# Kernel optimization log

Hardware: AMD Instinct MI355X
Metric: run time of the kernel (lower is better)

## Reference

```python
import jax, jax.numpy as jnp
import numpy as np

N_REUPLOADS = 3


def _qrun(x, Wp, bp, W1, b1, W2, b2):
    """Q-RUN layer: linear proj -> sin/cos reupload stack -> tiny per-channel MLP -> flatten.
    x: [..., in_dim]; Wp: [H2, in_dim]; W1: [mlp_h, 2*n_reuploads]; W2: [2, mlp_h].
    Returns [..., 2*H2].
    """
    p = jnp.einsum('...i,hi->...h', x, Wp) + bp                 # [..., H2]
    # features ordered [sin, cos, sin, cos, sin, cos] as in torch.stack of extend-ed list
    sc = jnp.stack([jnp.sin(p), jnp.cos(p)], axis=-1)           # [..., H2, 2]
    feats = jnp.tile(sc, (1,) * (sc.ndim - 1) + (N_REUPLOADS,))  # [..., H2, 6]
    h = jax.nn.relu(jnp.einsum('...k,mk->...m', feats, W1) + b1)  # [..., H2, 32]
    o = jnp.einsum('...m,om->...o', h, W2) + b2                 # [..., H2, 2]
    return o.reshape(o.shape[:-2] + (-1,))                      # flatten(start_dim=-2)


def setup_inputs() -> dict:
    key = jax.random.key(0)
    ks = jax.random.split(key, 20)
    H, I, MH, K = 5120, 27648, 32, 2 * N_REUPLOADS
    d = {}
    d['x'] = jax.random.normal(ks[0], (1, 256, H), dtype=jnp.float32)

    def mk(kbase, in_dim, out_half):
        k1, k2, k3, k4 = jax.random.split(kbase, 4)
        return (
            jax.random.normal(k1, (out_half, in_dim), jnp.float32) * (1.0 / np.sqrt(in_dim)),
            jnp.zeros((out_half,), jnp.float32),
            jax.random.normal(k2, (MH, K), jnp.float32) * 0.1,
            jnp.zeros((MH,), jnp.float32),
            jax.random.normal(k3, (2, MH), jnp.float32) * 0.01,
            jnp.zeros((2,), jnp.float32),
        )

    (d['Wg'], d['bg'], d['W1g'], d['b1g'], d['W2g'], d['b2g']) = mk(ks[1], H, I // 2)
    (d['Wu'], d['bu'], d['W1u'], d['b1u'], d['W2u'], d['b2u']) = mk(ks[2], H, I // 2)
    (d['Wd'], d['bd'], d['W1d'], d['b1d'], d['W2d'], d['b2d']) = mk(ks[3], I, H // 2)
    return d


def reference(x, Wg, bg, W1g, b1g, W2g, b2g,
              Wu, bu, W1u, b1u, W2u, b2u,
              Wd, bd, W1d, b1d, W2d, b2d):
    gate = _qrun(x, Wg, bg, W1g, b1g, W2g, b2g)   # [B,S,27648]
    up = _qrun(x, Wu, bu, W1u, b1u, W2u, b2u)     # [B,S,27648]
    h = jax.nn.silu(gate) * up
    return _qrun(h, Wd, bd, W1d, b1d, W2d, b2d)   # [B,S,5120]
```

## Files before the change

### kernel.cpp

```cpp
#include <hip/hip_runtime.h>
#include <stdint.h>

typedef unsigned short u16;
typedef __attribute__((ext_vector_type(8))) short short8;
typedef __attribute__((ext_vector_type(4))) float f32x4;

#define KGU  5120
#define HCOL 27648
#define NPD  2560
#define KD   27648
#define SPLITD 12
#define KCHD 2304
#define PEL (256*2560)

#define RB4   4
#define ABYT  16384
#define BBYT  16384
#define BUFB  32768

__device__ __forceinline__ void gl_lds16(const void* gp, void* lp) {
  __builtin_amdgcn_global_load_lds((const __attribute__((address_space(1))) uint32_t*)gp,
                                   (__attribute__((address_space(3))) uint32_t*)lp, 16, 0, 0);
}
__device__ __forceinline__ void gl_lds16nt(const void* gp, void* lp) {
  __builtin_amdgcn_global_load_lds((const __attribute__((address_space(1))) uint32_t*)gp,
                                   (__attribute__((address_space(3))) uint32_t*)lp, 16, 0, 2);
}
__device__ __forceinline__ uint32_t f2bf(float x) {
  uint32_t b = __float_as_uint(x);
  return (b + 0x7fffu + ((b >> 16) & 1u)) >> 16;
}
__device__ __forceinline__ uint32_t pk2(float lo, float hi) { return f2bf(lo) | (f2bf(hi) << 16); }
__device__ __forceinline__ float silu(float x) {
  return x * __builtin_amdgcn_rcpf(1.f + __expf(-x));
}
__device__ __forceinline__ short8 mk_bf8(const float4& a, const float4& b) {
  union { uint32_t u[4]; short8 s; } cv;
  cv.u[0] = pk2(a.x, a.y); cv.u[1] = pk2(a.z, a.w);
  cv.u[2] = pk2(b.x, b.y); cv.u[3] = pk2(b.z, b.w);
  return cv.s;
}

__global__ __launch_bounds__(256) void k_cvt(const float* __restrict__ X, u16* __restrict__ Xb) {
  int i = (blockIdx.x * 256 + threadIdx.x) * 8;
  float4 a = *(const float4*)(X + i);
  float4 b = *(const float4*)(X + i + 4);
  uint4 v;
  v.x = pk2(a.x, a.y); v.y = pk2(a.z, a.w); v.z = pk2(b.x, b.y); v.w = pk2(b.z, b.w);
  *(uint4*)(Xb + i) = v;
}

__global__ __launch_bounds__(512, 1)
void k_gu(const u16* __restrict__ X,
          const float* __restrict__ Wg, const float* __restrict__ bg,
          const float* __restrict__ W1g, const float* __restrict__ b1g,
          const float* __restrict__ W2g, const float* __restrict__ b2g,
          const float* __restrict__ Wu, const float* __restrict__ bu,
          const float* __restrict__ W1u, const float* __restrict__ b1u,
          const float* __restrict__ W2u, const float* __restrict__ b2u,
          u16* __restrict__ H) {
  __shared__ __align__(16) char smem[RB4 * BUFB + 1536];
  const int tid = threadIdx.x, lane = tid & 63, wid = tid >> 6;
  const int wm = wid >> 1, wn = wid & 1;
  const int s_ = lane & 15, quad = lane >> 4;
  const int j0 = blockIdx.x * 64;

  float4* mc4 = (float4*)(smem + RB4 * BUFB);
  float*  mc1 = (float*)(smem + RB4 * BUFB + 1024);
  if (tid < 64) {
    int sel = tid >> 5, m = tid & 31;
    const float* w1 = (sel ? W1u : W1g) + m * 6;
    const float* b1 = sel ? b1u : b1g;
    const float* w2 = sel ? W2u : W2g;
    mc4[sel * 32 + m] = make_float4(w1[0] + w1[2] + w1[4], w1[1] + w1[3] + w1[5], b1[m], w2[m]);
    mc1[sel * 32 + m] = w2[32 + m];
  }

  const u16* srcA0 = X + (size_t)(32 * wid + (lane & 15)) * KGU + (lane >> 4) * 8;
  const u16* srcA1 = srcA0 + 16 * KGU;
  const int jrow = j0 + 8 * wid + ((lane & 7) >> 1);
  const float* srcB0 = ((lane & 1) ? Wu : Wg) + (size_t)jrow * KGU + (lane >> 3) * 4;
  const float* srcB1 = srcB0 + 4 * KGU;
  const int dA0 = (2 * wid) * 1024, dA1 = dA0 + 1024;
  const int dB0 = ABYT + (2 * wid) * 1024, dB1 = dB0 + 1024;

  const int aoff0 = wm * 4096 + s_ * 16 + quad * 256;
  const int boff0 = ABYT + wn * 8192 + (s_ >> 3) * 1024 + (s_ & 7) * 16 + quad * 256;

  f32x4 acc[4][4];
#pragma unroll
  for (int i = 0; i < 4; ++i)
#pragma unroll
    for (int j = 0; j < 4; ++j) acc[i][j] = (f32x4)0.f;

  auto stage = [&](int bufb, int t) {
    const int kt = t * 32;
    gl_lds16(srcA0 + kt, smem + bufb + dA0);
    gl_lds16(srcA1 + kt, smem + bufb + dA1);
    gl_lds16nt(srcB0 + kt, smem + bufb + dB0);
    gl_lds16nt(srcB1 + kt, smem + bufb + dB1);
  };
  auto compute = [&](int bufb) {
    const char* base = smem + bufb;
    short8 af[4], bf[4];
#pragma unroll
    for (int mi = 0; mi < 4; ++mi)
      af[mi] = *(const short8*)(base + aoff0 + mi * 1024);
#pragma unroll
    for (int ni = 0; ni < 4; ++ni) {
      float4 f0 = *(const float4*)(base + boff0 + ni * 2048);
      float4 f1 = *(const float4*)(base + boff0 + ni * 2048 + 128);
      bf[ni] = mk_bf8(f0, f1);
    }
    __builtin_amdgcn_s_setprio(1);
#pragma unroll
    for (int mi = 0; mi < 4; ++mi)
#pragma unroll
      for (int ni = 0; ni < 4; ++ni)
        acc[mi][ni] = __builtin_amdgcn_mfma_f32_16x16x32_bf16(af[mi], bf[ni], acc[mi][ni], 0, 0, 0);
    __builtin_amdgcn_s_setprio(0);
  };

  stage(0, 0); stage(BUFB, 1);
#pragma unroll 1
  for (int t = 0; t < 158; ++t) {
    stage(((t + 2) & 3) * BUFB, t + 2);
    asm volatile("s_waitcnt vmcnt(8)" ::: "memory");
    __builtin_amdgcn_s_barrier();
    __builtin_amdgcn_sched_barrier(0);
    compute((t & 3) * BUFB);
  }
  asm volatile("s_waitcnt vmcnt(4)" ::: "memory");
  __builtin_amdgcn_s_barrier();
  __builtin_amdgcn_sched_barrier(0);
  compute((158 & 3) * BUFB);
  asm volatile("s_waitcnt vmcnt(0)" ::: "memory");
  __builtin_amdgcn_s_barrier();
  __builtin_amdgcn_sched_barrier(0);
  compute((159 & 3) * BUFB);

  __syncthreads();
  const int sel = lane & 1;
  const float b2v0 = sel ? b2u[0] : b2g[0];
  const float b2v1 = sel ? b2u[1] : b2g[1];
  const float4* mcs = mc4 + sel * 32;
  const float*  mcw = mc1 + sel * 32;
#pragma unroll
  for (int ni = 0; ni < 4; ++ni) {
    const int c = wn * 64 + ni * 16 + s_;
    const int j = j0 + (c >> 1);
    const float bp = sel ? bu[j] : bg[j];
#pragma unroll
    for (int mi = 0; mi < 4; ++mi) {
      float sv[4], cv[4], o0[4], o1[4];
#pragma unroll
      for (int e = 0; e < 4; ++e) {
        float p = acc[mi][ni][e] + bp;
        sv[e] = __sinf(p); cv[e] = __cosf(p);
        o0[e] = b2v0; o1[e] = b2v1;
      }
#pragma unroll 4
      for (int m = 0; m < 32; ++m) {
        float4 k4 = mcs[m]; float w2b = mcw[m];
#pragma unroll
        for (int e = 0; e < 4; ++e) {
          float hh = fmaxf(fmaf(sv[e], k4.x, fmaf(cv[e], k4.y, k4.z)), 0.f);
          o0[e] = fmaf(hh, k4.w, o0[e]);
          o1[e] = fmaf(hh, w2b, o1[e]);
        }
      }
#pragma unroll
      for (int e = 0; e < 4; ++e) {
        float t0 = __shfl_xor(o0[e], 1);
        float t1 = __shfl_xor(o1[e], 1);
        float g0 = sel ? t0 : o0[e];
        float u0 = sel ? o0[e] : t0;
        float g1 = sel ? t1 : o1[e];
        float u1 = sel ? o1[e] : t1;
        float h0 = silu(g0) * u0, h1 = silu(g1) * u1;
        if (!sel) {
          const int row = wm * 64 + mi * 16 + quad * 4 + e;
          *(uint32_t*)&H[(size_t)row * HCOL + 2 * j] = pk2(h0, h1);
        }
      }
    }
  }
}

__global__ __launch_bounds__(512, 1)
void k_down(const u16* __restrict__ Hb, const float* __restrict__ Wd, float* __restrict__ P2) {
  __shared__ __align__(16) char smem[RB4 * BUFB];
  const int tid = threadIdx.x, lane = tid & 63, wid = tid >> 6;
  const int wm = wid >> 1, wn = wid & 1;
  const int s_ = lane & 15, quad = lane >> 4;
  const int n0 = blockIdx.x * 128;
  const int kc = blockIdx.y * KCHD;

  const u16* srcA0 = Hb + (size_t)(32 * wid + (lane & 15)) * KD + kc + (lane >> 4) * 8;
  const u16* srcA1 = srcA0 + 16 * KD;
  const float* srcB0 = Wd + (size_t)(n0 + 16 * wid + (lane & 7)) * KD + kc + (lane >> 3) * 4;
  const float* srcB1 = srcB0 + 8 * KD;
  const int dA0 = (2 * wid) * 1024, dA1 = dA0 + 1024;
  const int dB0 = ABYT + (2 * wid) * 1024, dB1 = dB0 + 1024;

  const int aoff0 = wm * 4096 + s_ * 16 + quad * 256;
  const int boff0 = ABYT + wn * 8192 + (s_ >> 3) * 1024 + (s_ & 7) * 16 + quad * 256;

  f32x4 acc[4][4];
#pragma unroll
  for (int i = 0; i < 4; ++i)
#pragma unroll
    for (int j = 0; j < 4; ++j) acc[i][j] = (f32x4)0.f;

  auto stage = [&](int bufb, int t) {
    const int kt = t * 32;
    gl_lds16(srcA0 + kt, smem + bufb + dA0);
    gl_lds16(srcA1 + kt, smem + bufb + dA1);
    gl_lds16nt(srcB0 + kt, smem + bufb + dB0);
    gl_lds16nt(srcB1 + kt, smem + bufb + dB1);
  };
  auto compute = [&](int bufb) {
    const char* base = smem + bufb;
    short8 af[4], bf[4];
#pragma unroll
    for (int mi = 0; mi < 4; ++mi)
      af[mi] = *(const short8*)(base + aoff0 + mi * 1024);
#pragma unroll
    for (int ni = 0; ni < 4; ++ni) {
      float4 f0 = *(const float4*)(base + boff0 + ni * 2048);
      float4 f1 = *(const float4*)(base + boff0 + ni * 2048 + 128);
      bf[ni] = mk_bf8(f0, f1);
    }
    __builtin_amdgcn_s_setprio(1);
#pragma unroll
    for (int mi = 0; mi < 4; ++mi)
#pragma unroll
      for (int ni = 0; ni < 4; ++ni)
        acc[mi][ni] = __builtin_amdgcn_mfma_f32_16x16x32_bf16(af[mi], bf[ni], acc[mi][ni], 0, 0, 0);
    __builtin_amdgcn_s_setprio(0);
  };

  stage(0, 0); stage(BUFB, 1);
#pragma unroll 1
  for (int t = 0; t < 70; ++t) {
    stage(((t + 2) & 3) * BUFB, t + 2);
    asm volatile("s_waitcnt vmcnt(8)" ::: "memory");
    __builtin_amdgcn_s_barrier();
    __builtin_amdgcn_sched_barrier(0);
    compute((t & 3) * BUFB);
  }
  asm volatile("s_waitcnt vmcnt(4)" ::: "memory");
  __builtin_amdgcn_s_barrier();
  __builtin_amdgcn_sched_barrier(0);
  compute((70 & 3) * BUFB);
  asm volatile("s_waitcnt vmcnt(0)" ::: "memory");
  __builtin_amdgcn_s_barrier();
  __builtin_amdgcn_sched_barrier(0);
  compute((71 & 3) * BUFB);

  const size_t pb = (size_t)blockIdx.y * PEL;
#pragma unroll
  for (int mi = 0; mi < 4; ++mi) {
    int mrow = wm * 64 + mi * 16 + (quad << 2);
#pragma unroll
    for (int ni = 0; ni < 4; ++ni) {
      int n = n0 + wn * 64 + ni * 16 + s_;
#pragma unroll
      for (int e = 0; e < 4; ++e)
        P2[pb + (size_t)(mrow + e) * NPD + n] = acc[mi][ni][e];
    }
  }
}

__global__ __launch_bounds__(256) void k_fin(const float* __restrict__ P2, const float* __restrict__ bd,
    const float* __restrict__ W1d, const float* __restrict__ b1d, const float* __restrict__ W2d,
    const float* __restrict__ b2d, float* __restrict__ out) {
  __shared__ float4 mc0[32];
  __shared__ float mc1[32];
  const int tid = threadIdx.x;
  if (tid < 32) {
    const float* w = W1d + tid * 6;
    mc0[tid] = make_float4(w[0] + w[2] + w[4], w[1] + w[3] + w[5], b1d[tid], W2d[tid]);
    mc1[tid] = W2d[32 + tid];
  }
  __syncthreads();
  const int idx = blockIdx.x * 256 + tid;
  const int m = idx / NPD, j = idx - m * NPD;
  float p = bd[j];
#pragma unroll
  for (int sk = 0; sk < SPLITD; ++sk) p += P2[(size_t)sk * PEL + idx];
  float s = __sinf(p), c = __cosf(p);
  float o0 = b2d[0], o1 = b2d[1];
#pragma unroll 4
  for (int mm = 0; mm < 32; ++mm) {
    float4 k = mc0[mm];
    float hh = fmaxf(fmaf(s, k.x, fmaf(c, k.y, k.z)), 0.f);
    o0 = fmaf(hh, k.w, o0);
    o1 = fmaf(hh, mc1[mm], o1);
  }
  *(float2*)&out[(size_t)m * 5120 + 2 * j] = make_float2(o0, o1);
}

extern "C" void kernel_launch(void* const* d_in, const int* in_sizes, int n_in,
                              void* d_out, int out_size, void* d_ws, size_t ws_size,
                              hipStream_t stream) {
  const float* x   = (const float*)d_in[0];
  const float* Wg  = (const float*)d_in[1];
  const float* bg  = (const float*)d_in[2];
  const float* W1g = (const float*)d_in[3];
  const float* b1g = (const float*)d_in[4];
  const float* W2g = (const float*)d_in[5];
  const float* b2g = (const float*)d_in[6];
  const float* Wu  = (const float*)d_in[7];
  const float* bu  = (const float*)d_in[8];
  const float* W1u = (const float*)d_in[9];
  const float* b1u = (const float*)d_in[10];
  const float* W2u = (const float*)d_in[11];
  const float* b2u = (const float*)d_in[12];
  const float* Wd  = (const float*)d_in[13];
  const float* bd  = (const float*)d_in[14];
  const float* W1d = (const float*)d_in[15];
  const float* b1d = (const float*)d_in[16];
  const float* W2d = (const float*)d_in[17];
  const float* b2d = (const float*)d_in[18];
  char* ws = (char*)d_ws;
  u16*  xb = (u16*)ws;
  u16*  hb = (u16*)(ws + 2621440);
  float* P2 = (float*)(ws + 16777216);
  if (ws_size < 48234496u) return;

  k_cvt<<<dim3(640), dim3(256), 0, stream>>>(x, xb);
  k_gu<<<dim3(216), dim3(512), 0, stream>>>(xb, Wg, bg, W1g, b1g, W2g, b2g,
                                            Wu, bu, W1u, b1u, W2u, b2u, hb);
  k_down<<<dim3(20, SPLITD), dim3(512), 0, stream>>>(hb, Wd, P2);
  k_fin<<<dim3(2560), dim3(256), 0, stream>>>(P2, bd, W1d, b1d, W2d, b2d, (float*)d_out);
}
```

Measured before the change: 370.3 us.

## Convert fp32 weights to bf16 once in LDS with register-staged double buffering

The GEMM kernels stop copying fp32 weight tiles straight into LDS and converting them to bf16 in every wave. Each thread now loads its weight slice into registers, packs it with v_cvt_pk_bf16_f32, and writes a compact bf16 tile into a 2-stage LDS ring, so all waves share one conversion per element. Blocks shrink to 256 threads over 128 rows with 2 blocks per CU, which doubles the grids and halves LDS per block. The trade-off is a shallower pipeline (2 stages instead of 4) with a full wait on memory and a barrier every iteration, plus weight tiles re-read from memory by twice as many M-split blocks.

```diff
diff --git a/kernel.cpp b/kernel.cpp
--- a/kernel.cpp
+++ b/kernel.cpp
@@ -13,32 +13,25 @@
 #define KCHD 2304
 #define PEL (256*2560)
 
-#define RB4   4
-#define ABYT  16384
-#define BBYT  16384
-#define BUFB  32768
+#define BUF2 16384
+#define BOFF 8192
 
 __device__ __forceinline__ void gl_lds16(const void* gp, void* lp) {
   __builtin_amdgcn_global_load_lds((const __attribute__((address_space(1))) uint32_t*)gp,
                                    (__attribute__((address_space(3))) uint32_t*)lp, 16, 0, 0);
 }
-__device__ __forceinline__ void gl_lds16nt(const void* gp, void* lp) {
-  __builtin_amdgcn_global_load_lds((const __attribute__((address_space(1))) uint32_t*)gp,
-                                   (__attribute__((address_space(3))) uint32_t*)lp, 16, 0, 2);
-}
 __device__ __forceinline__ uint32_t f2bf(float x) {
   uint32_t b = __float_as_uint(x);
   return (b + 0x7fffu + ((b >> 16) & 1u)) >> 16;
 }
 __device__ __forceinline__ uint32_t pk2(float lo, float hi) { return f2bf(lo) | (f2bf(hi) << 16); }
+__device__ __forceinline__ uint32_t cvtpk(float lo, float hi) {
+  uint32_t r;
+  asm("v_cvt_pk_bf16_f32 %0, %1, %2" : "=v"(r) : "v"(lo), "v"(hi));
+  return r;
+}
 __device__ __forceinline__ float silu(float x) {
   return x * __builtin_amdgcn_rcpf(1.f + __expf(-x));
-}
-__device__ __forceinline__ short8 mk_bf8(const float4& a, const float4& b) {
-  union { uint32_t u[4]; short8 s; } cv;
-  cv.u[0] = pk2(a.x, a.y); cv.u[1] = pk2(a.z, a.w);
-  cv.u[2] = pk2(b.x, b.y); cv.u[3] = pk2(b.z, b.w);
-  return cv.s;
 }
 
 __global__ __launch_bounds__(256) void k_cvt(const float* __restrict__ X, u16* __restrict__ Xb) {
@@ -50,7 +43,7 @@
   *(uint4*)(Xb + i) = v;
 }
 
-__global__ __launch_bounds__(512, 1)
+__global__ __launch_bounds__(256, 2)
 void k_gu(const u16* __restrict__ X,
           const float* __restrict__ Wg, const float* __restrict__ bg,
           const float* __restrict__ W1g, const float* __restrict__ b1g,
@@ -59,14 +52,15 @@
           const float* __restrict__ W1u, const float* __restrict__ b1u,
           const float* __restrict__ W2u, const float* __restrict__ b2u,
           u16* __restrict__ H) {
-  __shared__ __align__(16) char smem[RB4 * BUFB + 1536];
+  __shared__ __align__(16) char smem[2 * BUF2 + 1536];
   const int tid = threadIdx.x, lane = tid & 63, wid = tid >> 6;
   const int wm = wid >> 1, wn = wid & 1;
   const int s_ = lane & 15, quad = lane >> 4;
-  const int j0 = blockIdx.x * 64;
-
-  float4* mc4 = (float4*)(smem + RB4 * BUFB);
-  float*  mc1 = (float*)(smem + RB4 * BUFB + 1024);
+  const int m0 = (blockIdx.x & 1) * 128;
+  const int j0 = (blockIdx.x >> 1) * 64;
+
+  float4* mc4 = (float4*)(smem + 2 * BUF2);
+  float*  mc1 = (float*)(smem + 2 * BUF2 + 1024);
   if (tid < 64) {
     int sel = tid >> 5, m = tid & 31;
     const float* w1 = (sel ? W1u : W1g) + m * 6;
@@ -76,16 +70,17 @@
     mc1[sel * 32 + m] = w2[32 + m];
   }
 
-  const u16* srcA0 = X + (size_t)(32 * wid + (lane & 15)) * KGU + (lane >> 4) * 8;
-  const u16* srcA1 = srcA0 + 16 * KGU;
-  const int jrow = j0 + 8 * wid + ((lane & 7) >> 1);
-  const float* srcB0 = ((lane & 1) ? Wu : Wg) + (size_t)jrow * KGU + (lane >> 3) * 4;
-  const float* srcB1 = srcB0 + 4 * KGU;
-  const int dA0 = (2 * wid) * 1024, dA1 = dA0 + 1024;
-  const int dB0 = ABYT + (2 * wid) * 1024, dB1 = dB0 + 1024;
-
-  const int aoff0 = wm * 4096 + s_ * 16 + quad * 256;
-  const int boff0 = ABYT + wn * 8192 + (s_ >> 3) * 1024 + (s_ & 7) * 16 + quad * 256;
+  const int c2 = wid * 2;
+  const u16* srcA0 = X + (size_t)(m0 + c2 * 16 + (lane >> 2)) * KGU + (lane & 3) * 8;
+  const u16* srcA1 = srcA0 + (size_t)16 * KGU;
+  const int dA0 = c2 * 1024, dA1 = dA0 + 1024;
+
+  const int br = tid >> 1, bh = tid & 1;
+  const float* srcB = ((br & 1) ? Wu : Wg) + (size_t)(j0 + (br >> 1)) * KGU + bh * 16;
+  const int bwr = BOFF + br * 64 + bh * 32;
+
+  const int aoff = (wm * 64 + s_) * 64 + quad * 16;
+  const int boff = BOFF + (wn * 64 + s_) * 64 + quad * 16;
 
   f32x4 acc[4][4];
 #pragma unroll
@@ -93,25 +88,33 @@
 #pragma unroll
     for (int j = 0; j < 4; ++j) acc[i][j] = (f32x4)0.f;
 
-  auto stage = [&](int bufb, int t) {
-    const int kt = t * 32;
-    gl_lds16(srcA0 + kt, smem + bufb + dA0);
-    gl_lds16(srcA1 + kt, smem + bufb + dA1);
-    gl_lds16nt(srcB0 + kt, smem + bufb + dB0);
-    gl_lds16nt(srcB1 + kt, smem + bufb + dB1);
-  };
-  auto compute = [&](int bufb) {
-    const char* base = smem + bufb;
+  float4 q0, q1, q2, q3;
+  auto loadB = [&](int kt) {
+    q0 = *(const float4*)(srcB + kt);
+    q1 = *(const float4*)(srcB + kt + 4);
+    q2 = *(const float4*)(srcB + kt + 8);
+    q3 = *(const float4*)(srcB + kt + 12);
+  };
+  auto stageA = [&](int buf, int kt) {
+    gl_lds16(srcA0 + kt, smem + buf + dA0);
+    gl_lds16(srcA1 + kt, smem + buf + dA1);
+  };
+  auto writeB = [&](int buf) {
+    uint4 v0, v1;
+    v0.x = cvtpk(q0.x, q0.y); v0.y = cvtpk(q0.z, q0.w);
+    v0.z = cvtpk(q1.x, q1.y); v0.w = cvtpk(q1.z, q1.w);
+    v1.x = cvtpk(q2.x, q2.y); v1.y = cvtpk(q2.z, q2.w);
+    v1.z = cvtpk(q3.x, q3.y); v1.w = cvtpk(q3.z, q3.w);
+    *(uint4*)(smem + buf + bwr) = v0;
+    *(uint4*)(smem + buf + bwr + 16) = v1;
+  };
+  auto compute = [&](int buf) {
+    const char* base = smem + buf;
     short8 af[4], bf[4];
 #pragma unroll
-    for (int mi = 0; mi < 4; ++mi)
-      af[mi] = *(const short8*)(base + aoff0 + mi * 1024);
-#pragma unroll
-    for (int ni = 0; ni < 4; ++ni) {
-      float4 f0 = *(const float4*)(base + boff0 + ni * 2048);
-      float4 f1 = *(const float4*)(base + boff0 + ni * 2048 + 128);
-      bf[ni] = mk_bf8(f0, f1);
-    }
+    for (int mi = 0; mi < 4; ++mi) af[mi] = *(const short8*)(base + aoff + mi * 1024);
+#pragma unroll
+    for (int ni = 0; ni < 4; ++ni) bf[ni] = *(const short8*)(base + boff + ni * 1024);
     __builtin_amdgcn_s_setprio(1);
 #pragma unroll
     for (int mi = 0; mi < 4; ++mi)
@@ -121,25 +124,31 @@
     __builtin_amdgcn_s_setprio(0);
   };
 
-  stage(0, 0); stage(BUFB, 1);
+  loadB(0); stageA(0, 0);
+  asm volatile("s_waitcnt vmcnt(2)" ::: "memory");
+  writeB(0);
+  asm volatile("s_waitcnt vmcnt(0) lgkmcnt(0)" ::: "memory");
+  __builtin_amdgcn_sched_barrier(0);
+  __builtin_amdgcn_s_barrier();
+  int cur = 0;
 #pragma unroll 1
-  for (int t = 0; t < 158; ++t) {
-    stage(((t + 2) & 3) * BUFB, t + 2);
-    asm volatile("s_waitcnt vmcnt(8)" ::: "memory");
+  for (int t = 0; t < 159; ++t) {
+    const int kt = (t + 1) * 32;
+    const int bo = cur << 14, bn = bo ^ BUF2;
+    loadB(kt);
+    stageA(bn, kt);
+    __builtin_amdgcn_sched_barrier(0);
+    compute(bo);
+    __builtin_amdgcn_sched_barrier(0);
+    asm volatile("s_waitcnt vmcnt(2)" ::: "memory");
+    writeB(bn);
+    asm volatile("s_waitcnt vmcnt(0) lgkmcnt(0)" ::: "memory");
+    __builtin_amdgcn_sched_barrier(0);
     __builtin_amdgcn_s_barrier();
-    __builtin_amdgcn_sched_barrier(0);
-    compute((t & 3) * BUFB);
-  }
-  asm volatile("s_waitcnt vmcnt(4)" ::: "memory");
-  __builtin_amdgcn_s_barrier();
-  __builtin_amdgcn_sched_barrier(0);
-  compute((158 & 3) * BUFB);
-  asm volatile("s_waitcnt vmcnt(0)" ::: "memory");
-  __builtin_amdgcn_s_barrier();
-  __builtin_amdgcn_sched_barrier(0);
-  compute((159 & 3) * BUFB);
-
-  __syncthreads();
+    cur ^= 1;
+  }
+  compute(cur << 14);
+
   const int sel = lane & 1;
   const float b2v0 = sel ? b2u[0] : b2g[0];
   const float b2v1 = sel ? b2u[1] : b2g[1];
@@ -179,7 +188,7 @@
         float u1 = sel ? o1[e] : t1;
         float h0 = silu(g0) * u0, h1 = silu(g1) * u1;
         if (!sel) {
-          const int row = wm * 64 + mi * 16 + quad * 4 + e;
+          const int row = m0 + wm * 64 + mi * 16 + quad * 4 + e;
           *(uint32_t*)&H[(size_t)row * HCOL + 2 * j] = pk2(h0, h1);
         }
       }
@@ -187,24 +196,27 @@
   }
 }
 
-__global__ __launch_bounds__(512, 1)
+__global__ __launch_bounds__(256, 2)
 void k_down(const u16* __restrict__ Hb, const float* __restrict__ Wd, float* __restrict__ P2) {
-  __shared__ __align__(16) char smem[RB4 * BUFB];
+  __shared__ __align__(16) char smem[2 * BUF2];
   const int tid = threadIdx.x, lane = tid & 63, wid = tid >> 6;
   const int wm = wid >> 1, wn = wid & 1;
   const int s_ = lane & 15, quad = lane >> 4;
-  const int n0 = blockIdx.x * 128;
+  const int m0 = (blockIdx.x & 1) * 128;
+  const int n0 = (blockIdx.x >> 1) * 128;
   const int kc = blockIdx.y * KCHD;
 
-  const u16* srcA0 = Hb + (size_t)(32 * wid + (lane & 15)) * KD + kc + (lane >> 4) * 8;
-  const u16* srcA1 = srcA0 + 16 * KD;
-  const float* srcB0 = Wd + (size_t)(n0 + 16 * wid + (lane & 7)) * KD + kc + (lane >> 3) * 4;
-  const float* srcB1 = srcB0 + 8 * KD;
-  const int dA0 = (2 * wid) * 1024, dA1 = dA0 + 1024;
-  const int dB0 = ABYT + (2 * wid) * 1024, dB1 = dB0 + 1024;
-
-  const int aoff0 = wm * 4096 + s_ * 16 + quad * 256;
-  const int boff0 = ABYT + wn * 8192 + (s_ >> 3) * 1024 + (s_ & 7) * 16 + quad * 256;
+  const int c2 = wid * 2;
+  const u16* srcA0 = Hb + (size_t)(m0 + c2 * 16 + (lane >> 2)) * KD + kc + (lane & 3) * 8;
+  const u16* srcA1 = srcA0 + (size_t)16 * KD;
+  const int dA0 = c2 * 1024, dA1 = dA0 + 1024;
+
+  const int br = tid >> 1, bh = tid & 1;
+  const float* srcB = Wd + (size_t)(n0 + br) * KD + kc + bh * 16;
+  const int bwr = BOFF + br * 64 + bh * 32;
+
+  const int aoff = (wm * 64 + s_) * 64 + quad * 16;
+  const int boff = BOFF + (wn * 64 + s_) * 64 + quad * 16;
 
   f32x4 acc[4][4];
 #pragma unroll
@@ -212,25 +224,33 @@
 #pragma unroll
     for (int j = 0; j < 4; ++j) acc[i][j] = (f32x4)0.f;
 
-  auto stage = [&](int bufb, int t) {
-    const int kt = t * 32;
-    gl_lds16(srcA0 + kt, smem + bufb + dA0);
-    gl_lds16(srcA1 + kt, smem + bufb + dA1);
-    gl_lds16nt(srcB0 + kt, smem + bufb + dB0);
-    gl_lds16nt(srcB1 + kt, smem + bufb + dB1);
-  };
-  auto compute = [&](int bufb) {
-    const char* base = smem + bufb;
+  float4 q0, q1, q2, q3;
+  auto loadB = [&](int kt) {
+    q0 = *(const float4*)(srcB + kt);
+    q1 = *(const float4*)(srcB + kt + 4);
+    q2 = *(const float4*)(srcB + kt + 8);
+    q3 = *(const float4*)(srcB + kt + 12);
+  };
+  auto stageA = [&](int buf, int kt) {
+    gl_lds16(srcA0 + kt, smem + buf + dA0);
+    gl_lds16(srcA1 + kt, smem + buf + dA1);
+  };
+  auto writeB = [&](int buf) {
+    uint4 v0, v1;
+    v0.x = cvtpk(q0.x, q0.y); v0.y = cvtpk(q0.z, q0.w);
+    v0.z = cvtpk(q1.x, q1.y); v0.w = cvtpk(q1.z, q1.w);
+    v1.x = cvtpk(q2.x, q2.y); v1.y = cvtpk(q2.z, q2.w);
+    v1.z = cvtpk(q3.x, q3.y); v1.w = cvtpk(q3.z, q3.w);
+    *(uint4*)(smem + buf + bwr) = v0;
+    *(uint4*)(smem + buf + bwr + 16) = v1;
+  };
+  auto compute = [&](int buf) {
+    const char* base = smem + buf;
     short8 af[4], bf[4];
 #pragma unroll
-    for (int mi = 0; mi < 4; ++mi)
-      af[mi] = *(const short8*)(base + aoff0 + mi * 1024);
-#pragma unroll
-    for (int ni = 0; ni < 4; ++ni) {
-      float4 f0 = *(const float4*)(base + boff0 + ni * 2048);
-      float4 f1 = *(const float4*)(base + boff0 + ni * 2048 + 128);
-      bf[ni] = mk_bf8(f0, f1);
-    }
+    for (int mi = 0; mi < 4; ++mi) af[mi] = *(const short8*)(base + aoff + mi * 1024);
+#pragma unroll
+    for (int ni = 0; ni < 4; ++ni) bf[ni] = *(const short8*)(base + boff + ni * 1024);
     __builtin_amdgcn_s_setprio(1);
 #pragma unroll
     for (int mi = 0; mi < 4; ++mi)
@@ -240,28 +260,35 @@
     __builtin_amdgcn_s_setprio(0);
   };
 
-  stage(0, 0); stage(BUFB, 1);
+  loadB(0); stageA(0, 0);
+  asm volatile("s_waitcnt vmcnt(2)" ::: "memory");
+  writeB(0);
+  asm volatile("s_waitcnt vmcnt(0) lgkmcnt(0)" ::: "memory");
+  __builtin_amdgcn_sched_barrier(0);
+  __builtin_amdgcn_s_barrier();
+  int cur = 0;
 #pragma unroll 1
-  for (int t = 0; t < 70; ++t) {
-    stage(((t + 2) & 3) * BUFB, t + 2);
-    asm volatile("s_waitcnt vmcnt(8)" ::: "memory");
+  for (int t = 0; t < 71; ++t) {
+    const int kt = (t + 1) * 32;
+    const int bo = cur << 14, bn = bo ^ BUF2;
+    loadB(kt);
+    stageA(bn, kt);
+    __builtin_amdgcn_sched_barrier(0);
+    compute(bo);
+    __builtin_amdgcn_sched_barrier(0);
+    asm volatile("s_waitcnt vmcnt(2)" ::: "memory");
+    writeB(bn);
+    asm volatile("s_waitcnt vmcnt(0) lgkmcnt(0)" ::: "memory");
+    __builtin_amdgcn_sched_barrier(0);
     __builtin_amdgcn_s_barrier();
-    __builtin_amdgcn_sched_barrier(0);
-    compute((t & 3) * BUFB);
-  }
-  asm volatile("s_waitcnt vmcnt(4)" ::: "memory");
-  __builtin_amdgcn_s_barrier();
-  __builtin_amdgcn_sched_barrier(0);
-  compute((70 & 3) * BUFB);
-  asm volatile("s_waitcnt vmcnt(0)" ::: "memory");
-  __builtin_amdgcn_s_barrier();
-  __builtin_amdgcn_sched_barrier(0);
-  compute((71 & 3) * BUFB);
+    cur ^= 1;
+  }
+  compute(cur << 14);
 
   const size_t pb = (size_t)blockIdx.y * PEL;
 #pragma unroll
   for (int mi = 0; mi < 4; ++mi) {
-    int mrow = wm * 64 + mi * 16 + (quad << 2);
+    int mrow = m0 + wm * 64 + mi * 16 + (quad << 2);
 #pragma unroll
     for (int ni = 0; ni < 4; ++ni) {
       int n = n0 + wn * 64 + ni * 16 + s_;
@@ -330,8 +357,8 @@
   if (ws_size < 48234496u) return;
 
   k_cvt<<<dim3(640), dim3(256), 0, stream>>>(x, xb);
-  k_gu<<<dim3(216), dim3(512), 0, stream>>>(xb, Wg, bg, W1g, b1g, W2g, b2g,
+  k_gu<<<dim3(432), dim3(256), 0, stream>>>(xb, Wg, bg, W1g, b1g, W2g, b2g,
                                             Wu, bu, W1u, b1u, W2u, b2u, hb);
-  k_down<<<dim3(20, SPLITD), dim3(512), 0, stream>>>(hb, Wd, P2);
+  k_down<<<dim3(40, SPLITD), dim3(256), 0, stream>>>(hb, Wd, P2);
   k_fin<<<dim3(2560), dim3(256), 0, stream>>>(P2, bd, W1d, b1d, W2d, b2d, (float*)d_out);
 }
```

New measurement: 418.8 us. 13.1% more time.

## Pre-swizzle activations into MFMA fragment layout and convert weights to bf16 once in LDS

Applied to the files above, without the earlier changes.

Activations X and H are now written in a fragment-major layout, so each lane loads its MFMA A operand straight from global memory and A no longer goes through LDS. Weight tiles are loaded into registers, converted to bf16 with v_cvt_pk_bf16_f32, and stored into a double-buffered, XOR-swizzled LDS tile. This replaces the fp32 LDS staging that was re-converted on every read. Grids are remapped with an XCD-aware block order, k_gu tiles are halved to 32 columns for more blocks, and launch bounds allow more blocks per CU. The risks are a shallower prefetch pipeline (register double buffering instead of four LDS stages) and A fragments fetched uncached from global memory.

```diff
diff --git a/kernel.cpp b/kernel.cpp
--- a/kernel.cpp
+++ b/kernel.cpp
@@ -6,67 +6,62 @@
 typedef __attribute__((ext_vector_type(4))) float f32x4;
 
 #define KGU  5120
-#define HCOL 27648
 #define NPD  2560
 #define KD   27648
 #define SPLITD 12
 #define KCHD 2304
 #define PEL (256*2560)
 
-#define RB4   4
-#define ABYT  16384
-#define BBYT  16384
-#define BUFB  32768
-
-__device__ __forceinline__ void gl_lds16(const void* gp, void* lp) {
-  __builtin_amdgcn_global_load_lds((const __attribute__((address_space(1))) uint32_t*)gp,
-                                   (__attribute__((address_space(3))) uint32_t*)lp, 16, 0, 0);
-}
-__device__ __forceinline__ void gl_lds16nt(const void* gp, void* lp) {
-  __builtin_amdgcn_global_load_lds((const __attribute__((address_space(1))) uint32_t*)gp,
-                                   (__attribute__((address_space(3))) uint32_t*)lp, 16, 0, 2);
-}
 __device__ __forceinline__ uint32_t f2bf(float x) {
   uint32_t b = __float_as_uint(x);
   return (b + 0x7fffu + ((b >> 16) & 1u)) >> 16;
 }
 __device__ __forceinline__ uint32_t pk2(float lo, float hi) { return f2bf(lo) | (f2bf(hi) << 16); }
+__device__ __forceinline__ uint32_t cvtpk(float lo, float hi) {
+  uint32_t r;
+  asm("v_cvt_pk_bf16_f32 %0, %1, %2" : "=v"(r) : "v"(lo), "v"(hi));
+  return r;
+}
 __device__ __forceinline__ float silu(float x) {
   return x * __builtin_amdgcn_rcpf(1.f + __expf(-x));
 }
-__device__ __forceinline__ short8 mk_bf8(const float4& a, const float4& b) {
-  union { uint32_t u[4]; short8 s; } cv;
-  cv.u[0] = pk2(a.x, a.y); cv.u[1] = pk2(a.z, a.w);
-  cv.u[2] = pk2(b.x, b.y); cv.u[3] = pk2(b.z, b.w);
-  return cv.s;
-}
-
-__global__ __launch_bounds__(256) void k_cvt(const float* __restrict__ X, u16* __restrict__ Xb) {
-  int i = (blockIdx.x * 256 + threadIdx.x) * 8;
-  float4 a = *(const float4*)(X + i);
-  float4 b = *(const float4*)(X + i + 4);
-  uint4 v;
-  v.x = pk2(a.x, a.y); v.y = pk2(a.z, a.w); v.z = pk2(b.x, b.y); v.w = pk2(b.z, b.w);
-  *(uint4*)(Xb + i) = v;
-}
-
-__global__ __launch_bounds__(512, 1)
-void k_gu(const u16* __restrict__ X,
+#define MFMA16(a,b,c) __builtin_amdgcn_mfma_f32_16x16x32_bf16(a, b, c, 0, 0, 0)
+
+__global__ __launch_bounds__(256) void k_cvt(const float* __restrict__ X, u16* __restrict__ XF) {
+  const int kt = blockIdx.x;
+  const int lane = threadIdx.x & 63, wv = threadIdx.x >> 6;
+#pragma unroll
+  for (int ii = 0; ii < 4; ++ii) {
+    const int mt = wv * 4 + ii;
+    const float* src = X + (size_t)(mt * 16 + (lane & 15)) * KGU + kt * 32 + (lane >> 4) * 8;
+    float4 f0 = *(const float4*)src;
+    float4 f1 = *(const float4*)(src + 4);
+    uint4 v;
+    v.x = cvtpk(f0.x, f0.y); v.y = cvtpk(f0.z, f0.w);
+    v.z = cvtpk(f1.x, f1.y); v.w = cvtpk(f1.z, f1.w);
+    *(uint4*)(XF + ((size_t)(kt * 16 + mt) * 64 + lane) * 8) = v;
+  }
+}
+
+__global__ __launch_bounds__(512, 4)
+void k_gu(const u16* __restrict__ XF,
           const float* __restrict__ Wg, const float* __restrict__ bg,
           const float* __restrict__ W1g, const float* __restrict__ b1g,
           const float* __restrict__ W2g, const float* __restrict__ b2g,
           const float* __restrict__ Wu, const float* __restrict__ bu,
           const float* __restrict__ W1u, const float* __restrict__ b1u,
           const float* __restrict__ W2u, const float* __restrict__ b2u,
-          u16* __restrict__ H) {
-  __shared__ __align__(16) char smem[RB4 * BUFB + 1536];
+          u16* __restrict__ HF) {
+  __shared__ __align__(16) char smem[66560];
   const int tid = threadIdx.x, lane = tid & 63, wid = tid >> 6;
   const int wm = wid >> 1, wn = wid & 1;
   const int s_ = lane & 15, quad = lane >> 4;
-  const int j0 = blockIdx.x * 64;
-
-  float4* mc4 = (float4*)(smem + RB4 * BUFB);
-  float*  mc1 = (float*)(smem + RB4 * BUFB + 1024);
+  const int bx = blockIdx.x;
+  const int w = (bx & 7) * 54 + (bx >> 3);
+  const int j0p = w * 32;
+
+  float4* mc4 = (float4*)(smem + 65536);
+  float*  mc1 = (float*)(smem + 65536 + 1024);
   if (tid < 64) {
     int sel = tid >> 5, m = tid & 31;
     const float* w1 = (sel ? W1u : W1g) + m * 6;
@@ -76,79 +71,77 @@
     mc1[sel * 32 + m] = w2[32 + m];
   }
 
-  const u16* srcA0 = X + (size_t)(32 * wid + (lane & 15)) * KGU + (lane >> 4) * 8;
-  const u16* srcA1 = srcA0 + 16 * KGU;
-  const int jrow = j0 + 8 * wid + ((lane & 7) >> 1);
-  const float* srcB0 = ((lane & 1) ? Wu : Wg) + (size_t)jrow * KGU + (lane >> 3) * 4;
-  const float* srcB1 = srcB0 + 4 * KGU;
-  const int dA0 = (2 * wid) * 1024, dA1 = dA0 + 1024;
-  const int dB0 = ABYT + (2 * wid) * 1024, dB1 = dB0 + 1024;
-
-  const int aoff0 = wm * 4096 + s_ * 16 + quad * 256;
-  const int boff0 = ABYT + wn * 8192 + (s_ >> 3) * 1024 + (s_ & 7) * 16 + quad * 256;
-
-  f32x4 acc[4][4];
-#pragma unroll
-  for (int i = 0; i < 4; ++i)
-#pragma unroll
-    for (int j = 0; j < 4; ++j) acc[i][j] = (f32x4)0.f;
-
-  auto stage = [&](int bufb, int t) {
-    const int kt = t * 32;
-    gl_lds16(srcA0 + kt, smem + bufb + dA0);
-    gl_lds16(srcA1 + kt, smem + bufb + dA1);
-    gl_lds16nt(srcB0 + kt, smem + bufb + dB0);
-    gl_lds16nt(srcB1 + kt, smem + bufb + dB1);
-  };
-  auto compute = [&](int bufb) {
-    const char* base = smem + bufb;
-    short8 af[4], bf[4];
-#pragma unroll
-    for (int mi = 0; mi < 4; ++mi)
-      af[mi] = *(const short8*)(base + aoff0 + mi * 1024);
-#pragma unroll
-    for (int ni = 0; ni < 4; ++ni) {
-      float4 f0 = *(const float4*)(base + boff0 + ni * 2048);
-      float4 f1 = *(const float4*)(base + boff0 + ni * 2048 + 128);
-      bf[ni] = mk_bf8(f0, f1);
-    }
-    __builtin_amdgcn_s_setprio(1);
-#pragma unroll
-    for (int mi = 0; mi < 4; ++mi)
-#pragma unroll
-      for (int ni = 0; ni < 4; ++ni)
-        acc[mi][ni] = __builtin_amdgcn_mfma_f32_16x16x32_bf16(af[mi], bf[ni], acc[mi][ni], 0, 0, 0);
-    __builtin_amdgcn_s_setprio(0);
-  };
-
-  stage(0, 0); stage(BUFB, 1);
+  const int kkl = lane >> 3;
+  const int s0 = 8 * (wid & 1);
+  const int wbase = kkl * 4096 + (wid >> 1) * 1024 + ((lane >> 1) & 3) * 256 + (lane & 1) * 8;
+  const float* srcG = Wg + (size_t)(j0p + 4 * wid) * KGU + 4 * lane;
+  const float* srcU = Wu + (size_t)(j0p + 4 * wid) * KGU + 4 * lane;
+
+  const int rbase = quad * 256 + (s_ << 4);
+  const short8* XFp = (const short8*)XF;
+
+  f32x4 acc[4][2];
+#pragma unroll
+  for (int i = 0; i < 4; ++i) { acc[i][0] = (f32x4)0.f; acc[i][1] = (f32x4)0.f; }
+
+  float4 sr[8];
+#pragma unroll
+  for (int i = 0; i < 8; ++i) {
+    const float* p = ((i & 1) ? srcU : srcG) + (size_t)(i >> 1) * KGU;
+    sr[i] = *(const float4*)p;
+  }
+
 #pragma unroll 1
-  for (int t = 0; t < 158; ++t) {
-    stage(((t + 2) & 3) * BUFB, t + 2);
-    asm volatile("s_waitcnt vmcnt(8)" ::: "memory");
+  for (int st = 0; st < 20; ++st) {
+    char* buf = smem + (st & 1) * 32768;
+#pragma unroll
+    for (int i = 0; i < 8; ++i) {
+      uint2 v; v.x = cvtpk(sr[i].x, sr[i].y); v.y = cvtpk(sr[i].z, sr[i].w);
+      *(uint2*)(buf + wbase + (((s0 + i) ^ kkl) << 4)) = v;
+    }
+    __builtin_amdgcn_sched_barrier(0);
+    if (st < 19) {
+      const int kf = (st + 1) * 256;
+#pragma unroll
+      for (int i = 0; i < 8; ++i) {
+        const float* p = ((i & 1) ? srcU : srcG) + (size_t)(i >> 1) * KGU + kf;
+        sr[i] = *(const float4*)p;
+      }
+    }
+    __builtin_amdgcn_sched_barrier(0);
+    asm volatile("s_waitcnt lgkmcnt(0)" ::: "memory");
     __builtin_amdgcn_s_barrier();
     __builtin_amdgcn_sched_barrier(0);
-    compute((t & 3) * BUFB);
-  }
-  asm volatile("s_waitcnt vmcnt(4)" ::: "memory");
-  __builtin_amdgcn_s_barrier();
-  __builtin_amdgcn_sched_barrier(0);
-  compute((158 & 3) * BUFB);
-  asm volatile("s_waitcnt vmcnt(0)" ::: "memory");
-  __builtin_amdgcn_s_barrier();
-  __builtin_amdgcn_sched_barrier(0);
-  compute((159 & 3) * BUFB);
-
-  __syncthreads();
+    const short8* pa = XFp + ((size_t)(st * 8) * 16 + wm * 4) * 64 + lane;
+    const char* bb = buf + (wn * 2) * 1024;
+#pragma unroll
+    for (int kk = 0; kk < 8; ++kk) {
+      short8 a0 = pa[(kk * 16 + 0) * 64];
+      short8 a1 = pa[(kk * 16 + 1) * 64];
+      short8 a2 = pa[(kk * 16 + 2) * 64];
+      short8 a3 = pa[(kk * 16 + 3) * 64];
+      const int ro = kk * 4096 + (rbase ^ (kk << 4));
+      short8 b0 = *(const short8*)(bb + ro);
+      short8 b1 = *(const short8*)(bb + ro + 1024);
+      __builtin_amdgcn_s_setprio(1);
+      acc[0][0] = MFMA16(a0, b0, acc[0][0]); acc[0][1] = MFMA16(a0, b1, acc[0][1]);
+      acc[1][0] = MFMA16(a1, b0, acc[1][0]); acc[1][1] = MFMA16(a1, b1, acc[1][1]);
+      acc[2][0] = MFMA16(a2, b0, acc[2][0]); acc[2][1] = MFMA16(a2, b1, acc[2][1]);
+      acc[3][0] = MFMA16(a3, b0, acc[3][0]); acc[3][1] = MFMA16(a3, b1, acc[3][1]);
+      __builtin_amdgcn_s_setprio(0);
+    }
+  }
+
   const int sel = lane & 1;
   const float b2v0 = sel ? b2u[0] : b2g[0];
   const float b2v1 = sel ? b2u[1] : b2g[1];
   const float4* mcs = mc4 + sel * 32;
   const float*  mcw = mc1 + sel * 32;
-#pragma unroll
-  for (int ni = 0; ni < 4; ++ni) {
-    const int c = wn * 64 + ni * 16 + s_;
-    const int j = j0 + (c >> 1);
+  char* HFb = (char*)HF;
+#pragma unroll
+  for (int ni = 0; ni < 2; ++ni) {
+    const int c = wn * 32 + ni * 16 + s_;
+    const int j = j0p + (c >> 1);
     const float bp = sel ? bu[j] : bg[j];
 #pragma unroll
     for (int mi = 0; mi < 4; ++mi) {
@@ -180,31 +173,35 @@
         float h0 = silu(g0) * u0, h1 = silu(g1) * u1;
         if (!sel) {
           const int row = wm * 64 + mi * 16 + quad * 4 + e;
-          *(uint32_t*)&H[(size_t)row * HCOL + 2 * j] = pk2(h0, h1);
+          const int kt2 = j >> 4, mt2 = wm * 4 + mi;
+          const int lf2 = (row & 15) + 16 * ((j >> 2) & 3);
+          *(uint32_t*)(HFb + (size_t)(kt2 * 16 + mt2) * 1024 + lf2 * 16 + (j & 3) * 4)
+              = pk2(h0, h1);
         }
       }
     }
   }
 }
 
-__global__ __launch_bounds__(512, 1)
-void k_down(const u16* __restrict__ Hb, const float* __restrict__ Wd, float* __restrict__ P2) {
-  __shared__ __align__(16) char smem[RB4 * BUFB];
+__global__ __launch_bounds__(512, 2)
+void k_down(const u16* __restrict__ HF, const float* __restrict__ Wd, float* __restrict__ P2) {
+  __shared__ __align__(16) char smem[65536];
   const int tid = threadIdx.x, lane = tid & 63, wid = tid >> 6;
   const int wm = wid >> 1, wn = wid & 1;
   const int s_ = lane & 15, quad = lane >> 4;
-  const int n0 = blockIdx.x * 128;
-  const int kc = blockIdx.y * KCHD;
-
-  const u16* srcA0 = Hb + (size_t)(32 * wid + (lane & 15)) * KD + kc + (lane >> 4) * 8;
-  const u16* srcA1 = srcA0 + 16 * KD;
-  const float* srcB0 = Wd + (size_t)(n0 + 16 * wid + (lane & 7)) * KD + kc + (lane >> 3) * 4;
-  const float* srcB1 = srcB0 + 8 * KD;
-  const int dA0 = (2 * wid) * 1024, dA1 = dA0 + 1024;
-  const int dB0 = ABYT + (2 * wid) * 1024, dB1 = dB0 + 1024;
-
-  const int aoff0 = wm * 4096 + s_ * 16 + quad * 256;
-  const int boff0 = ABYT + wn * 8192 + (s_ >> 3) * 1024 + (s_ & 7) * 16 + quad * 256;
+  const int bx = blockIdx.x;
+  const int w = (bx & 7) * 30 + (bx >> 3);
+  const int sk = w / 20, nt = w % 20;
+  const int n0 = nt * 128;
+  const int kc = sk * KCHD;
+
+  const int b5 = lane >> 5;
+  const float* srcD = Wd + (size_t)(n0 + 16 * wid + b5) * KD + kc + 4 * (lane & 31);
+  const int kkd = (lane & 31) >> 3;
+  const int wbase = kkd * 8192 + wid * 1024 + ((lane & 7) >> 1) * 256 + (lane & 1) * 8;
+  const int rbase = quad * 256 + (s_ << 4);
+  const short8* HFp = (const short8*)HF;
+  const int kc32 = sk * 72;
 
   f32x4 acc[4][4];
 #pragma unroll
@@ -212,53 +209,56 @@
 #pragma unroll
     for (int j = 0; j < 4; ++j) acc[i][j] = (f32x4)0.f;
 
-  auto stage = [&](int bufb, int t) {
-    const int kt = t * 32;
-    gl_lds16(srcA0 + kt, smem + bufb + dA0);
-    gl_lds16(srcA1 + kt, smem + bufb + dA1);
-    gl_lds16nt(srcB0 + kt, smem + bufb + dB0);
-    gl_lds16nt(srcB1 + kt, smem + bufb + dB1);
-  };
-  auto compute = [&](int bufb) {
-    const char* base = smem + bufb;
-    short8 af[4], bf[4];
-#pragma unroll
-    for (int mi = 0; mi < 4; ++mi)
-      af[mi] = *(const short8*)(base + aoff0 + mi * 1024);
-#pragma unroll
-    for (int ni = 0; ni < 4; ++ni) {
-      float4 f0 = *(const float4*)(base + boff0 + ni * 2048);
-      float4 f1 = *(const float4*)(base + boff0 + ni * 2048 + 128);
-      bf[ni] = mk_bf8(f0, f1);
-    }
-    __builtin_amdgcn_s_setprio(1);
-#pragma unroll
-    for (int mi = 0; mi < 4; ++mi)
-#pragma unroll
-      for (int ni = 0; ni < 4; ++ni)
-        acc[mi][ni] = __builtin_amdgcn_mfma_f32_16x16x32_bf16(af[mi], bf[ni], acc[mi][ni], 0, 0, 0);
-    __builtin_amdgcn_s_setprio(0);
-  };
-
-  stage(0, 0); stage(BUFB, 1);
+  float4 sr[8];
+#pragma unroll
+  for (int i = 0; i < 8; ++i) sr[i] = *(const float4*)(srcD + (size_t)(2 * i) * KD);
+
 #pragma unroll 1
-  for (int t = 0; t < 70; ++t) {
-    stage(((t + 2) & 3) * BUFB, t + 2);
-    asm volatile("s_waitcnt vmcnt(8)" ::: "memory");
+  for (int st = 0; st < 18; ++st) {
+    char* buf = smem + (st & 1) * 32768;
+#pragma unroll
+    for (int i = 0; i < 8; ++i) {
+      uint2 v; v.x = cvtpk(sr[i].x, sr[i].y); v.y = cvtpk(sr[i].z, sr[i].w);
+      *(uint2*)(buf + wbase + (((2 * i + b5) ^ kkd) << 4)) = v;
+    }
+    __builtin_amdgcn_sched_barrier(0);
+    if (st < 17) {
+      const int kf = (st + 1) * 128;
+#pragma unroll
+      for (int i = 0; i < 8; ++i)
+        sr[i] = *(const float4*)(srcD + (size_t)(2 * i) * KD + kf);
+    }
+    __builtin_amdgcn_sched_barrier(0);
+    asm volatile("s_waitcnt lgkmcnt(0)" ::: "memory");
     __builtin_amdgcn_s_barrier();
     __builtin_amdgcn_sched_barrier(0);
-    compute((t & 3) * BUFB);
-  }
-  asm volatile("s_waitcnt vmcnt(4)" ::: "memory");
-  __builtin_amdgcn_s_barrier();
-  __builtin_amdgcn_sched_barrier(0);
-  compute((70 & 3) * BUFB);
-  asm volatile("s_waitcnt vmcnt(0)" ::: "memory");
-  __builtin_amdgcn_s_barrier();
-  __builtin_amdgcn_sched_barrier(0);
-  compute((71 & 3) * BUFB);
-
-  const size_t pb = (size_t)blockIdx.y * PEL;
+    const short8* pa = HFp + ((size_t)(kc32 + st * 4) * 16 + wm * 4) * 64 + lane;
+    const char* bb = buf + (wn * 4) * 1024;
+#pragma unroll
+    for (int kk = 0; kk < 4; ++kk) {
+      short8 a0 = pa[(kk * 16 + 0) * 64];
+      short8 a1 = pa[(kk * 16 + 1) * 64];
+      short8 a2 = pa[(kk * 16 + 2) * 64];
+      short8 a3 = pa[(kk * 16 + 3) * 64];
+      const int ro = kk * 8192 + (rbase ^ (kk << 4));
+      short8 b0 = *(const short8*)(bb + ro);
+      short8 b1 = *(const short8*)(bb + ro + 1024);
+      short8 b2 = *(const short8*)(bb + ro + 2048);
+      short8 b3 = *(const short8*)(bb + ro + 3072);
+      __builtin_amdgcn_s_setprio(1);
+      acc[0][0] = MFMA16(a0, b0, acc[0][0]); acc[0][1] = MFMA16(a0, b1, acc[0][1]);
+      acc[0][2] = MFMA16(a0, b2, acc[0][2]); acc[0][3] = MFMA16(a0, b3, acc[0][3]);
+      acc[1][0] = MFMA16(a1, b0, acc[1][0]); acc[1][1] = MFMA16(a1, b1, acc[1][1]);
+      acc[1][2] = MFMA16(a1, b2, acc[1][2]); acc[1][3] = MFMA16(a1, b3, acc[1][3]);
+      acc[2][0] = MFMA16(a2, b0, acc[2][0]); acc[2][1] = MFMA16(a2, b1, acc[2][1]);
+      acc[2][2] = MFMA16(a2, b2, acc[2][2]); acc[2][3] = MFMA16(a2, b3, acc[2][3]);
+      acc[3][0] = MFMA16(a3, b0, acc[3][0]); acc[3][1] = MFMA16(a3, b1, acc[3][1]);
+      acc[3][2] = MFMA16(a3, b2, acc[3][2]); acc[3][3] = MFMA16(a3, b3, acc[3][3]);
+      __builtin_amdgcn_s_setprio(0);
+    }
+  }
+
+  const size_t pb = (size_t)sk * PEL;
 #pragma unroll
   for (int mi = 0; mi < 4; ++mi) {
     int mrow = wm * 64 + mi * 16 + (quad << 2);
@@ -324,14 +324,14 @@
   const float* W2d = (const float*)d_in[17];
   const float* b2d = (const float*)d_in[18];
   char* ws = (char*)d_ws;
-  u16*  xb = (u16*)ws;
-  u16*  hb = (u16*)(ws + 2621440);
+  u16*  XF = (u16*)ws;
+  u16*  HF = (u16*)(ws + 2621440);
   float* P2 = (float*)(ws + 16777216);
   if (ws_size < 48234496u) return;
 
-  k_cvt<<<dim3(640), dim3(256), 0, stream>>>(x, xb);
-  k_gu<<<dim3(216), dim3(512), 0, stream>>>(xb, Wg, bg, W1g, b1g, W2g, b2g,
-                                            Wu, bu, W1u, b1u, W2u, b2u, hb);
-  k_down<<<dim3(20, SPLITD), dim3(512), 0, stream>>>(hb, Wd, P2);
+  k_cvt<<<dim3(160), dim3(256), 0, stream>>>(x, XF);
+  k_gu<<<dim3(432), dim3(512), 0, stream>>>(XF, Wg, bg, W1g, b1g, W2g, b2g,
+                                            Wu, bu, W1u, b1u, W2u, b2u, HF);
+  k_down<<<dim3(240), dim3(512), 0, stream>>>(HF, Wd, P2);
   k_fin<<<dim3(2560), dim3(256), 0, stream>>>(P2, bd, W1d, b1d, W2d, b2d, (float*)d_out);
 }
```

Result: faster. 299.6 us (-19.1%).
